# Performance work log

Hardware: AMD Instinct MI355X
Metric: run time of the kernel (lower is better)

Reference implementation:

```python
import jax, jax.numpy as jnp
import numpy as np

B, DIN, H, NACT = 8192, 1025, 1024, 1026
NHEAD = 513  # npatches + STOP
K = 32       # kR = kS


def _make_seq(key, batch, n, k):
    k_idx, k_len = jax.random.split(key)
    # distinct indices per row: top-k of a random permutation
    perm = jnp.argsort(jax.random.uniform(k_idx, (batch, n)), axis=1)[:, :k]
    seq_len = jax.random.randint(k_len, (batch,), 1, k + 1).astype(jnp.int32)
    mask = jnp.arange(k)[None, :] < seq_len[:, None]
    seq_idx = jnp.where(mask, perm, -1).astype(jnp.int32)
    return seq_idx, seq_len


def setup_inputs() -> dict:
    key = jax.random.key(0)
    ks = jax.random.split(key, 8)
    state = jax.random.normal(ks[0], (B, DIN), dtype=jnp.float32)
    W0 = jax.random.normal(ks[1], (DIN, H), dtype=jnp.float32) * (2.0 / DIN) ** 0.5
    b0 = jnp.zeros((H,), jnp.float32)
    W1 = jax.random.normal(ks[2], (H, H), dtype=jnp.float32) * (2.0 / H) ** 0.5
    b1 = jnp.zeros((H,), jnp.float32)
    W2 = jax.random.normal(ks[3], (H, NACT), dtype=jnp.float32) * 0.01
    b2 = jnp.zeros((NACT,), jnp.float32)
    seq_idx_R, seq_len_R = _make_seq(ks[4], B, NHEAD, K)
    seq_idx_S, seq_len_S = _make_seq(ks[5], B, NHEAD, K)
    return {"state": state, "W0": W0, "b0": b0, "W1": W1, "b1": b1,
            "W2": W2, "b2": b2,
            "seq_idx_R": seq_idx_R, "seq_len_R": seq_len_R,
            "seq_idx_S": seq_idx_S, "seq_len_S": seq_len_S}


def _mlp(state, W0, b0, W1, b1, W2, b2):
    h = jax.nn.relu(state @ W0 + b0)
    h = jax.nn.relu(h @ W1 + b1)
    return h @ W2 + b2  # (B, NACT) logits


def _logprob_entropy_wo_replacement(logits, seq_idx, seq_len):
    # Faithful vectorized version of logprob_entropy_wo_replacement_batched.
    bsz, n = logits.shape
    col = jnp.arange(n)[None, :]
    neg_inf = jnp.float32(-jnp.inf)

    def step(carry, xs):
        remaining, logp, ent = carry          # (B,N) bool, (B,), (B,)
        t, idx_t = xs                          # scalar, (B,)
        active = t < seq_len                   # (B,)
        masked_logits = jnp.where(remaining, logits, neg_inf)
        lp = jax.nn.log_softmax(masked_logits, axis=-1)
        p = jnp.exp(lp)
        mp = jnp.where(remaining, p, 0.0)
        mlp_ = jnp.where(remaining, lp, 0.0)
        ent_step = -jnp.sum(mp * mlp_, axis=-1)
        ent = ent + jnp.where(active, ent_step, 0.0)
        valid = active & (idx_t >= 0)
        idx_safe = jnp.where(valid, idx_t, 0)
        g = jnp.take_along_axis(lp, idx_safe[:, None], axis=1)[:, 0]
        logp = logp + jnp.where(valid, g, 0.0)
        hit = (col == idx_safe[:, None]) & valid[:, None]
        remaining = remaining & ~hit
        return (remaining, logp, ent), None

    init = (jnp.ones((bsz, n), bool), jnp.zeros((bsz,), jnp.float32),
            jnp.zeros((bsz,), jnp.float32))
    ts = jnp.arange(seq_idx.shape[1], dtype=jnp.int32)
    (_, logp, ent), _ = jax.lax.scan(step, init, (ts, seq_idx.T))
    return logp, ent


def reference(state, W0, b0, W1, b1, W2, b2,
              seq_idx_R, seq_len_R, seq_idx_S, seq_len_S):
    x = _mlp(state, W0, b0, W1, b1, W2, b2)
    logpR, entR = _logprob_entropy_wo_replacement(x[:, :NHEAD], seq_idx_R, seq_len_R)
    logpS, entS = _logprob_entropy_wo_replacement(x[:, NHEAD:NHEAD + NHEAD], seq_idx_S, seq_len_S)
    # rows: [total logprob, total entropy] as in get_log_prob's (logpR+logpS, entR+entS)
    return jnp.stack([logpR + logpS, entR + entS], axis=0)  # (2, B)
```

## Files before the change

kernel.cpp:

```cpp
#include <hip/hip_runtime.h>
#include <cstdint>
#include <cstddef>

#define BATCH 8192
#define DIN   1025
#define HID   1024
#define NACT  1026
#define NHEAD 513
#define KSEL  32
#define KP0   1088
#define LGN   1024

typedef unsigned short u16;
typedef short bf16x8 __attribute__((ext_vector_type(8)));
typedef float f32x4 __attribute__((ext_vector_type(4)));

__device__ __forceinline__ u16 f2bf(float f) {
  unsigned u = __float_as_uint(f);
  u += 0x7fff + ((u >> 16) & 1);
  return (u16)(u >> 16);
}
__device__ __forceinline__ float bf2f(u16 h) {
  return __uint_as_float((unsigned)h << 16);
}

__device__ __forceinline__ void async_cp16(const u16* g, u16* l) {
  __builtin_amdgcn_global_load_lds((const __attribute__((address_space(1))) void*)g,
                                   (__attribute__((address_space(3))) void*)l,
                                   16, 0, 0);
}

__global__ __launch_bounds__(512) void k_cvt(const float* __restrict__ state,
    const float* __restrict__ W0, const float* __restrict__ W1,
    const float* __restrict__ W2,
    u16* __restrict__ As, u16* __restrict__ W0t, u16* __restrict__ W1t,
    u16* __restrict__ W2t, u16* __restrict__ W2c) {
  const int tid = threadIdx.x;
  const int b = blockIdx.x;
  {
    int i = b * 512 + tid;
    const int QPR = KP0 / 4;
    int r = i / QPR, c4 = (i - r * QPR) * 4;
    const float* src = state + (size_t)r * DIN + c4;
    ushort4 o;
    if (c4 + 3 < DIN) {
      o.x = f2bf(src[0]); o.y = f2bf(src[1]); o.z = f2bf(src[2]); o.w = f2bf(src[3]);
    } else {
      o.x = (c4 + 0 < DIN) ? f2bf(src[0]) : 0;
      o.y = (c4 + 1 < DIN) ? f2bf(src[1]) : 0;
      o.z = (c4 + 2 < DIN) ? f2bf(src[2]) : 0;
      o.w = (c4 + 3 < DIN) ? f2bf(src[3]) : 0;
    }
    *(ushort4*)(As + (size_t)r * KP0 + c4) = o;
  }
  if (b >= 3137) return;
  if (b == 3136) {
    for (int e = tid; e < 2048; e += 512) {
      int j = e >> 10, k = e & 1023;
      W2c[e] = f2bf(W2[(size_t)k * NACT + 1024 + j]);
    }
    return;
  }
  const float* W; u16* Wt; int K, ldW, Kp, tt = b;
  if (tt < 1088)      { W = W0; Wt = W0t; K = DIN; ldW = HID;  Kp = KP0; }
  else if (tt < 2112) { tt -= 1088; W = W1; Wt = W1t; K = HID; ldW = HID;  Kp = HID; }
  else                { tt -= 2112; W = W2; Wt = W2t; K = HID; ldW = NACT; Kp = HID; }
  int n0 = (tt & 31) * 32, k0 = (tt >> 5) * 32;
  __shared__ float tile[32][33];
  const int tx = tid & 31, ty = tid >> 5;
#pragma unroll
  for (int i = 0; i < 32; i += 16) {
    int k = k0 + ty + i;
    tile[ty + i][tx] = (k < K) ? W[(size_t)k * ldW + n0 + tx] : 0.f;
  }
  __syncthreads();
#pragma unroll
  for (int i = 0; i < 32; i += 16)
    Wt[(size_t)(n0 + ty + i) * Kp + k0 + tx] = f2bf(tile[tx][ty + i]);
}

template<bool RELU, int K>
__global__ __launch_bounds__(512, 2)
void gemm_bt(const u16* __restrict__ A, const u16* __restrict__ Bt,
             const float* __restrict__ bias, u16* __restrict__ Cout, int ldc)
{
  __shared__ __align__(16) u16 lds[24576];

  const int d     = blockIdx.x;
  const int m8    = d & 7;
  const int ntile = (d >> 3) & 3;
  const int mtile = ((d >> 5) << 3) | m8;
  const size_t bm = (size_t)mtile * 128;
  const size_t bn = (size_t)ntile * 256;

  const int tid  = threadIdx.x;
  const int wave = tid >> 6;
  const int lane = tid & 63;
  const int waveM = wave >> 2, waveN = wave & 3;
  const int lr = lane & 15, lq = lane >> 4;

  const int rowA  = tid >> 2;
  const int gA_   = (tid & 3) ^ ((rowA >> 1) & 3);
  const int rowB0 = tid >> 2;
  const int gB0_  = (tid & 3) ^ ((rowB0 >> 1) & 3);
  const int rowB1 = rowB0 + 128;
  const int gB1_  = (tid & 3) ^ ((rowB1 >> 1) & 3);
  const u16* gA  = A  + (bm + rowA)  * (size_t)K + gA_  * 8;
  const u16* gB0 = Bt + (bn + rowB0) * (size_t)K + gB0_ * 8;
  const u16* gB1 = Bt + (bn + rowB1) * (size_t)K + gB1_ * 8;
  u16* lA  = lds + wave * 512;
  u16* lB0 = lds + 4096 + wave * 512;
  u16* lB1 = lB0 + 4096;

  f32x4 acc[4][4] = {};

  const int s = lq ^ ((lr >> 1) & 3);
  const u16* pa = lds + (waveM * 64 + lr) * 32 + s * 8;
  const u16* pb = lds + 4096 + (waveN * 64 + lr) * 32 + s * 8;

  auto issue = [&](int k0, int buf) {
    const int o = buf * 12288;
    async_cp16(gA  + k0, lA  + o);
    async_cp16(gB0 + k0, lB0 + o);
    async_cp16(gB1 + k0, lB1 + o);
  };

  const int NIT = K / 32;
  issue(0, 0);
#pragma unroll 2
  for (int it = 0; it < NIT; ++it) {
    const int buf = it & 1;
    if (it + 1 < NIT) {
      issue((it + 1) * 32, buf ^ 1);
      asm volatile("s_waitcnt vmcnt(3)\n\ts_barrier" ::: "memory");
    } else {
      asm volatile("s_waitcnt vmcnt(0)\n\ts_barrier" ::: "memory");
    }

    bf16x8 af[4], bf[4];
    const u16* qa = pa + buf * 12288;
    const u16* qb = pb + buf * 12288;
#pragma unroll
    for (int t = 0; t < 4; ++t) {
      af[t] = *(const bf16x8*)(qa + t * 512);
      bf[t] = *(const bf16x8*)(qb + t * 512);
    }
#pragma unroll
    for (int tm = 0; tm < 4; ++tm)
#pragma unroll
      for (int tn = 0; tn < 4; ++tn)
        acc[tm][tn] = __builtin_amdgcn_mfma_f32_16x16x32_bf16(af[tm], bf[tn], acc[tm][tn], 0, 0, 0);

    asm volatile("s_waitcnt lgkmcnt(0)\n\ts_barrier" ::: "memory");
  }

#pragma unroll
  for (int tm = 0; tm < 4; ++tm) {
    size_t rw = bm + waveM * 64 + tm * 16 + lq * 4;
#pragma unroll
    for (int tn = 0; tn < 4; ++tn) {
      int col = (int)bn + waveN * 64 + tn * 16 + lr;
      float bv = bias[col];
#pragma unroll
      for (int r = 0; r < 4; ++r) {
        float v = acc[tm][tn][r] + bv;
        if (RELU) v = fmaxf(v, 0.f);
        Cout[(rw + r) * ldc + col] = f2bf(v);
      }
    }
  }
}

__global__ __launch_bounds__(512) void k_sample(const u16* __restrict__ lgts,
    const u16* __restrict__ h2, const u16* __restrict__ W2c,
    const float* __restrict__ b2,
    const int* __restrict__ idxR, const int* __restrict__ lenR,
    const int* __restrict__ idxS, const int* __restrict__ lenS,
    float* __restrict__ out) {
  __shared__ float shf[16];
  const int tid = threadIdx.x;
  const int w = tid >> 6, lane = tid & 63;
  const int grp = w & 1, pair = w >> 1;
  const int row = blockIdx.x * 4 + pair;
  const u16* base = lgts + (size_t)row * LGN + (grp ? NHEAD : 0);
  const int* sidx = (grp ? idxS : idxR) + (size_t)row * KSEL;
  const int slen  = (grp ? lenS : lenR)[row];

  float x1024 = 0.f, x1025 = 0.f;
  if (grp) {
    float d0 = 0.f, d1 = 0.f;
    const u16* hr  = h2 + (size_t)row * HID + lane * 16;
    const u16* w0p = W2c + lane * 16;
    const u16* w1p = W2c + 1024 + lane * 16;
#pragma unroll
    for (int j = 0; j < 16; ++j) {
      float h = bf2f(hr[j]);
      d0 += h * bf2f(w0p[j]);
      d1 += h * bf2f(w1p[j]);
    }
#pragma unroll
    for (int dd = 32; dd; dd >>= 1) { d0 += __shfl_xor(d0, dd, 64); d1 += __shfl_xor(d1, dd, 64); }
    x1024 = d0 + b2[1024];
    x1025 = d1 + b2[1025];
  }
  const int NHm = grp ? 511 : 513;

  float m = -3.4e38f;
  for (int i = lane; i < NHm; i += 64) m = fmaxf(m, bf2f(base[i]));
  if (grp) {
    if (lane == 63) m = fmaxf(m, x1024);
    if (lane == 0)  m = fmaxf(m, x1025);
  }
#pragma unroll
  for (int dd = 32; dd; dd >>= 1) m = fmaxf(m, __shfl_xor(m, dd, 64));

  float S = 0.f, T = 0.f;
  for (int i = lane; i < NHm; i += 64) {
    float xi = bf2f(base[i]);
    float e = __expf(xi - m);
    S += e; T += e * xi;
  }
  if (grp) {
    if (lane == 63) { float e = __expf(x1024 - m); S += e; T += e * x1024; }
    if (lane == 0)  { float e = __expf(x1025 - m); S += e; T += e * x1025; }
  }
#pragma unroll
  for (int dd = 32; dd; dd >>= 1) { S += __shfl_xor(S, dd, 64); T += __shfl_xor(T, dd, 64); }

  float e = 0.f, ex = 0.f, xt = 0.f;
  int active = (lane < KSEL) && (lane < slen);
  int valid = 0;
  if (active) {
    int id = sidx[lane];
    if (id >= 0) {
      valid = 1;
      if (grp && id >= 511) xt = (id == 511) ? x1024 : x1025;
      else                  xt = bf2f(base[id]);
      e  = __expf(xt - m);
      ex = e * xt;
    }
  }
  float pe = e, pex = ex;
#pragma unroll
  for (int dd = 1; dd < 32; dd <<= 1) {
    float qa = __shfl_up(pe, dd, 64);
    float qb = __shfl_up(pex, dd, 64);
    if (lane >= dd) { pe += qa; pex += qb; }
  }
  float lp = 0.f, en = 0.f;
  if (active) {
    float St = S - (pe - e);
    float Tt = T - (pex - ex);
    float logZ = m + __logf(St);
    en = logZ - Tt / St;
    if (valid) lp = xt - logZ;
  }
#pragma unroll
  for (int dd = 32; dd; dd >>= 1) { lp += __shfl_xor(lp, dd, 64); en += __shfl_xor(en, dd, 64); }

  if (lane == 0) { shf[w * 2] = lp; shf[w * 2 + 1] = en; }
  __syncthreads();
  if (lane == 0 && grp == 0) {
    out[row]         = shf[pair * 4] + shf[pair * 4 + 2];
    out[BATCH + row] = shf[pair * 4 + 1] + shf[pair * 4 + 3];
  }
}

extern "C" void kernel_launch(void* const* d_in, const int* in_sizes, int n_in,
                              void* d_out, int out_size, void* d_ws, size_t ws_size,
                              hipStream_t stream) {
  (void)in_sizes; (void)n_in; (void)out_size; (void)ws_size;
  const float* state = (const float*)d_in[0];
  const float* W0 = (const float*)d_in[1];
  const float* b0 = (const float*)d_in[2];
  const float* W1 = (const float*)d_in[3];
  const float* b1 = (const float*)d_in[4];
  const float* W2 = (const float*)d_in[5];
  const float* b2 = (const float*)d_in[6];
  const int* idxR = (const int*)d_in[7];
  const int* lenR = (const int*)d_in[8];
  const int* idxS = (const int*)d_in[9];
  const int* lenS = (const int*)d_in[10];
  float* out = (float*)d_out;

  char* ws = (char*)d_ws;
  size_t off = 0;
  auto alloc = [&](size_t bytes) -> char* {
    char* p = ws + off;
    off = (off + bytes + 255) & ~(size_t)255;
    return p;
  };
  u16* As   = (u16*)alloc((size_t)BATCH * KP0 * 2);
  u16* W0t  = (u16*)alloc((size_t)HID * KP0 * 2);
  u16* W1t  = (u16*)alloc((size_t)HID * HID * 2);
  u16* W2t  = (u16*)alloc((size_t)HID * LGN * 2);
  u16* W2c  = (u16*)alloc((size_t)2 * 1024 * 2);
  u16* h1   = (u16*)alloc((size_t)BATCH * HID * 2);
  u16* h2   = (u16*)alloc((size_t)BATCH * HID * 2);
  u16* lgts = (u16*)alloc((size_t)BATCH * LGN * 2);

  k_cvt<<<4352, 512, 0, stream>>>(state, W0, W1, W2, As, W0t, W1t, W2t, W2c);

  gemm_bt<true,  KP0><<<256, 512, 0, stream>>>(As, W0t, b0, h1,   HID);
  gemm_bt<true,  HID><<<256, 512, 0, stream>>>(h1, W1t, b1, h2,   HID);
  gemm_bt<false, HID><<<256, 512, 0, stream>>>(h2, W2t, b2, lgts, LGN);

  k_sample<<<2048, 512, 0, stream>>>(lgts, h2, W2c, b2, idxR, lenR, idxS, lenS, out);
}
```

Before: 195.0 us.

## Shrink GEMM tiles to 128x128 with 256 threads and vectorize sampler loads

The GEMM blocks change from 128x256 tiles with 8 waves to 128x128 tiles with 4 waves. This doubles the grid to 512 blocks so the work covers more CUs, while per-block LDS use drops. The sampling kernel now reads each row's logits as a single 16-byte vector per lane instead of strided scalar loops, and also vectorizes the h2·W2 dot products for the last two columns. The trade-off is that smaller GEMM tiles lower operand reuse per block and add global traffic.

Result: faster. 185.9 us (-4.7%).

```diff
diff --git a/kernel.cpp b/kernel.cpp
--- a/kernel.cpp
+++ b/kernel.cpp
@@ -80,37 +80,36 @@
 }
 
 template<bool RELU, int K>
-__global__ __launch_bounds__(512, 2)
+__global__ __launch_bounds__(256, 2)
 void gemm_bt(const u16* __restrict__ A, const u16* __restrict__ Bt,
              const float* __restrict__ bias, u16* __restrict__ Cout, int ldc)
 {
-  __shared__ __align__(16) u16 lds[24576];
+  __shared__ __align__(16) u16 lds[16384];
 
   const int d     = blockIdx.x;
   const int m8    = d & 7;
-  const int ntile = (d >> 3) & 3;
-  const int mtile = ((d >> 5) << 3) | m8;
+  const int ntile = (d >> 3) & 7;
+  const int mtile = ((d >> 6) << 3) | m8;
   const size_t bm = (size_t)mtile * 128;
-  const size_t bn = (size_t)ntile * 256;
+  const size_t bn = (size_t)ntile * 128;
 
   const int tid  = threadIdx.x;
   const int wave = tid >> 6;
   const int lane = tid & 63;
-  const int waveM = wave >> 2, waveN = wave & 3;
+  const int waveM = wave >> 1, waveN = wave & 1;
   const int lr = lane & 15, lq = lane >> 4;
 
-  const int rowA  = tid >> 2;
-  const int gA_   = (tid & 3) ^ ((rowA >> 1) & 3);
-  const int rowB0 = tid >> 2;
-  const int gB0_  = (tid & 3) ^ ((rowB0 >> 1) & 3);
-  const int rowB1 = rowB0 + 128;
-  const int gB1_  = (tid & 3) ^ ((rowB1 >> 1) & 3);
-  const u16* gA  = A  + (bm + rowA)  * (size_t)K + gA_  * 8;
-  const u16* gB0 = Bt + (bn + rowB0) * (size_t)K + gB0_ * 8;
-  const u16* gB1 = Bt + (bn + rowB1) * (size_t)K + gB1_ * 8;
-  u16* lA  = lds + wave * 512;
+  const int row0 = tid >> 2;
+  const int row1 = row0 + 64;
+  const int g_   = (tid & 3) ^ ((tid >> 3) & 3);
+  const u16* gA0 = A  + (bm + row0) * (size_t)K + g_ * 8;
+  const u16* gA1 = A  + (bm + row1) * (size_t)K + g_ * 8;
+  const u16* gB0 = Bt + (bn + row0) * (size_t)K + g_ * 8;
+  const u16* gB1 = Bt + (bn + row1) * (size_t)K + g_ * 8;
+  u16* lA0 = lds + wave * 512;
+  u16* lA1 = lds + 2048 + wave * 512;
   u16* lB0 = lds + 4096 + wave * 512;
-  u16* lB1 = lB0 + 4096;
+  u16* lB1 = lds + 6144 + wave * 512;
 
   f32x4 acc[4][4] = {};
 
@@ -119,8 +118,9 @@
   const u16* pb = lds + 4096 + (waveN * 64 + lr) * 32 + s * 8;
 
   auto issue = [&](int k0, int buf) {
-    const int o = buf * 12288;
-    async_cp16(gA  + k0, lA  + o);
+    const int o = buf * 8192;
+    async_cp16(gA0 + k0, lA0 + o);
+    async_cp16(gA1 + k0, lA1 + o);
     async_cp16(gB0 + k0, lB0 + o);
     async_cp16(gB1 + k0, lB1 + o);
   };
@@ -132,24 +132,24 @@
     const int buf = it & 1;
     if (it + 1 < NIT) {
       issue((it + 1) * 32, buf ^ 1);
-      asm volatile("s_waitcnt vmcnt(3)\n\ts_barrier" ::: "memory");
+      asm volatile("s_waitcnt vmcnt(4)\n\ts_barrier" ::: "memory");
     } else {
       asm volatile("s_waitcnt vmcnt(0)\n\ts_barrier" ::: "memory");
     }
 
-    bf16x8 af[4], bf[4];
-    const u16* qa = pa + buf * 12288;
-    const u16* qb = pb + buf * 12288;
+    bf16x8 af[4], bfr[4];
+    const u16* qa = pa + buf * 8192;
+    const u16* qb = pb + buf * 8192;
 #pragma unroll
     for (int t = 0; t < 4; ++t) {
-      af[t] = *(const bf16x8*)(qa + t * 512);
-      bf[t] = *(const bf16x8*)(qb + t * 512);
+      af[t]  = *(const bf16x8*)(qa + t * 512);
+      bfr[t] = *(const bf16x8*)(qb + t * 512);
     }
 #pragma unroll
     for (int tm = 0; tm < 4; ++tm)
 #pragma unroll
       for (int tn = 0; tn < 4; ++tn)
-        acc[tm][tn] = __builtin_amdgcn_mfma_f32_16x16x32_bf16(af[tm], bf[tn], acc[tm][tn], 0, 0, 0);
+        acc[tm][tn] = __builtin_amdgcn_mfma_f32_16x16x32_bf16(af[tm], bfr[tn], acc[tm][tn], 0, 0, 0);
 
     asm volatile("s_waitcnt lgkmcnt(0)\n\ts_barrier" ::: "memory");
   }
@@ -188,42 +188,52 @@
 
   float x1024 = 0.f, x1025 = 0.f;
   if (grp) {
+    const bf16x8* hp  = (const bf16x8*)(h2 + (size_t)row * HID + lane * 16);
+    const bf16x8* w0p = (const bf16x8*)(W2c + lane * 16);
+    const bf16x8* w1p = (const bf16x8*)(W2c + 1024 + lane * 16);
+    bf16x8 hv0 = hp[0],  hv1 = hp[1];
+    bf16x8 a0  = w0p[0], a1  = w0p[1];
+    bf16x8 c0  = w1p[0], c1  = w1p[1];
     float d0 = 0.f, d1 = 0.f;
-    const u16* hr  = h2 + (size_t)row * HID + lane * 16;
-    const u16* w0p = W2c + lane * 16;
-    const u16* w1p = W2c + 1024 + lane * 16;
-#pragma unroll
-    for (int j = 0; j < 16; ++j) {
-      float h = bf2f(hr[j]);
-      d0 += h * bf2f(w0p[j]);
-      d1 += h * bf2f(w1p[j]);
+#pragma unroll
+    for (int j = 0; j < 8; ++j) {
+      float h0 = bf2f((u16)hv0[j]);
+      float h1 = bf2f((u16)hv1[j]);
+      d0 += h0 * bf2f((u16)a0[j]) + h1 * bf2f((u16)a1[j]);
+      d1 += h0 * bf2f((u16)c0[j]) + h1 * bf2f((u16)c1[j]);
     }
 #pragma unroll
     for (int dd = 32; dd; dd >>= 1) { d0 += __shfl_xor(d0, dd, 64); d1 += __shfl_xor(d1, dd, 64); }
     x1024 = d0 + b2[1024];
     x1025 = d1 + b2[1025];
   }
-  const int NHm = grp ? 511 : 513;
+
+  const u16* chunk = lgts + (size_t)row * LGN + (grp ? 512 : 0) + lane * 8;
+  bf16x8 raw = *(const bf16x8*)chunk;
+  float v[8];
+#pragma unroll
+  for (int j = 0; j < 8; ++j) v[j] = bf2f((u16)raw[j]);
+  if (grp && lane == 0) v[0] = -3.4e38f;
+
+  float xa = -3.4e38f; int has_xa = 0;
+  if (!grp && lane == 0)  { xa = bf2f(base[512]); has_xa = 1; }
+  if (grp  && lane == 63) { xa = x1024;           has_xa = 1; }
+  if (grp  && lane == 0)  { xa = x1025;           has_xa = 1; }
 
   float m = -3.4e38f;
-  for (int i = lane; i < NHm; i += 64) m = fmaxf(m, bf2f(base[i]));
-  if (grp) {
-    if (lane == 63) m = fmaxf(m, x1024);
-    if (lane == 0)  m = fmaxf(m, x1025);
-  }
+#pragma unroll
+  for (int j = 0; j < 8; ++j) m = fmaxf(m, v[j]);
+  if (has_xa) m = fmaxf(m, xa);
 #pragma unroll
   for (int dd = 32; dd; dd >>= 1) m = fmaxf(m, __shfl_xor(m, dd, 64));
 
   float S = 0.f, T = 0.f;
-  for (int i = lane; i < NHm; i += 64) {
-    float xi = bf2f(base[i]);
-    float e = __expf(xi - m);
-    S += e; T += e * xi;
-  }
-  if (grp) {
-    if (lane == 63) { float e = __expf(x1024 - m); S += e; T += e * x1024; }
-    if (lane == 0)  { float e = __expf(x1025 - m); S += e; T += e * x1025; }
-  }
+#pragma unroll
+  for (int j = 0; j < 8; ++j) {
+    float e = __expf(v[j] - m);
+    S += e; T += e * v[j];
+  }
+  if (has_xa) { float e = __expf(xa - m); S += e; T += e * xa; }
 #pragma unroll
   for (int dd = 32; dd; dd >>= 1) { S += __shfl_xor(S, dd, 64); T += __shfl_xor(T, dd, 64); }
 
@@ -301,9 +311,9 @@
 
   k_cvt<<<4352, 512, 0, stream>>>(state, W0, W1, W2, As, W0t, W1t, W2t, W2c);
 
-  gemm_bt<true,  KP0><<<256, 512, 0, stream>>>(As, W0t, b0, h1,   HID);
-  gemm_bt<true,  HID><<<256, 512, 0, stream>>>(h1, W1t, b1, h2,   HID);
-  gemm_bt<false, HID><<<256, 512, 0, stream>>>(h2, W2t, b2, lgts, LGN);
+  gemm_bt<true,  KP0><<<512, 256, 0, stream>>>(As, W0t, b0, h1,   HID);
+  gemm_bt<true,  HID><<<512, 256, 0, stream>>>(h1, W1t, b1, h2,   HID);
+  gemm_bt<false, HID><<<512, 256, 0, stream>>>(h2, W2t, b2, lgts, LGN);
 
   k_sample<<<2048, 512, 0, stream>>>(lgts, h2, W2c, b2, idxR, lenR, idxS, lenS, out);
 }
```
